# Performance work log

Hardware: AMD Instinct MI355X
Metric: run time of the kernel (lower is better)

The kernel has to match this reference:

```python
import jax, jax.numpy as jnp
import numpy as np

BLOCK = 32          # Q4_0 block size
Q_ZERO = 8.0        # 4-bit zero point


def setup_inputs() -> dict:
    key = jax.random.key(0)
    k1, k2, k3, k4 = jax.random.split(key, 4)
    O, I = 8192, 8192
    nb = I // BLOCK                      # 256 blocks per row
    x = jax.random.normal(k1, (4096, I), dtype=jnp.float32)
    # packed Q4_0 payload: 16 bytes per block, each byte holds two 4-bit quants
    qweight = jax.random.randint(k2, (O, nb, BLOCK // 2), 0, 256, dtype=jnp.int32)
    scales = jax.random.uniform(k3, (O, nb), dtype=jnp.float32)
    bias = jax.random.normal(k4, (O,), dtype=jnp.float32)
    return {"x": x, "qweight": qweight, "scales": scales, "bias": bias}


def _dequantize_q4_0(qweight, scales):
    # qweight: [O, NB, 16] bytes; low nibble -> elems 0..15, high nibble -> 16..31
    O, nb, _ = qweight.shape
    low = qweight & 0xF
    high = (qweight >> 4) & 0xF
    vals = jnp.concatenate([low, high], axis=-1).astype(scales.dtype)  # [O, NB, 32]
    w = (vals - Q_ZERO) * scales[..., None]                            # [O, NB, 32]
    return w.reshape(O, nb * BLOCK)                                    # [O, I]


def reference(x, qweight, scales, bias):
    # GGUFLayer.cast_bias_weight: dequantize weight/bias to input dtype, then linear
    w = _dequantize_q4_0(qweight, scales).astype(x.dtype)  # [O, I]
    b = bias.astype(x.dtype)
    return jnp.einsum('ni,oi->no', x, w) + b               # F.linear(x, w, b)
```

## Files before the change

kernel.cpp:

```cpp
#include <hip/hip_runtime.h>
#include <stdint.h>

#define M_DIM 4096
#define N_DIM 8192
#define K_DIM 8192
#define NB    256

#define BM 256
#define BN 256
#define BK 64

typedef __attribute__((ext_vector_type(8)))  __bf16 bf16x8;
typedef __attribute__((ext_vector_type(16))) float  floatx16;
typedef __attribute__((ext_vector_type(4)))  unsigned short ushort4v;
typedef __attribute__((ext_vector_type(8)))  unsigned short ushort8;

__device__ __forceinline__ unsigned short f32_to_bf16_rne(float f) {
    union { float f; unsigned int u; } v; v.f = f;
    unsigned int u = v.u;
    u += 0x7FFFu + ((u >> 16) & 1u);
    return (unsigned short)(u >> 16);
}

__global__ __launch_bounds__(256) void prep(const int* __restrict__ qw,
                                            const float* __restrict__ sc,
                                            unsigned short* __restrict__ w,
                                            const float* __restrict__ x,
                                            unsigned short* __restrict__ xb) {
    const int bid = blockIdx.x;
    if (bid & 1) {
        size_t idx = ((size_t)(bid >> 1) * 256 + threadIdx.x) * 4;
        float4 f = *(const float4*)(x + idx);
        ushort4v o;
        o[0] = f32_to_bf16_rne(f.x); o[1] = f32_to_bf16_rne(f.y);
        o[2] = f32_to_bf16_rne(f.z); o[3] = f32_to_bf16_rne(f.w);
        *(ushort4v*)(xb + idx) = o;
    } else {
        const int tid = (bid >> 1) * 256 + threadIdx.x;
        const int blk = tid >> 2;
        const int q   = tid & 3;
        const int4* src = (const int4*)qw + (size_t)blk * 4 + (q & 1) * 2;
        int4 v0 = src[0];
        int4 v1 = src[1];
        const float scale = sc[blk];
        const int sh = (q >> 1) * 4;
        int by[8] = { v0.x, v0.y, v0.z, v0.w, v1.x, v1.y, v1.z, v1.w };
        ushort8 o;
#pragma unroll
        for (int j = 0; j < 8; ++j)
            o[j] = f32_to_bf16_rne((float)(((by[j] >> sh) & 0xF) - 8) * scale);
        *(ushort8*)(w + (size_t)blk * 32 + q * 8) = o;
    }
}

__device__ __forceinline__ void load_lds16(const unsigned short* g, unsigned short* l) {
    __builtin_amdgcn_global_load_lds(
        (const __attribute__((address_space(1))) unsigned int*)(g),
        (__attribute__((address_space(3))) unsigned int*)(l),
        16, 0, 0);
}

__device__ __forceinline__ floatx16 mfma_op(bf16x8 a, bf16x8 b, floatx16 c) {
    return __builtin_amdgcn_mfma_f32_32x32x16_bf16(a, b, c, 0, 0, 0);
}

#define SL(kk, F) (((((kk) * 2) + q5) ^ (F)) * 8)

#define STAGE_A(b, h, kb) do { \
    load_lds16(gA + (size_t)((h) * 128 +  0) * K_DIM + (kb) * BK, &lsA[b][((h) * 128 +  0 + wave * 8) * BK]); \
    load_lds16(gA + (size_t)((h) * 128 + 64) * K_DIM + (kb) * BK, &lsA[b][((h) * 128 + 64 + wave * 8) * BK]); \
} while (0)
#define STAGE_B(b, h, kb) do { \
    load_lds16(gB + (size_t)((h) * 128 +  0) * K_DIM + (kb) * BK, &lsB[b][((h) * 128 +  0 + wave * 8) * BK]); \
    load_lds16(gB + (size_t)((h) * 128 + 64) * K_DIM + (kb) * BK, &lsB[b][((h) * 128 + 64 + wave * 8) * BK]); \
} while (0)

#define PH_HEAD __builtin_amdgcn_s_barrier(); \
                asm volatile("s_waitcnt lgkmcnt(0)" ::: "memory"); \
                __builtin_amdgcn_s_setprio(1)
#define PH_TAIL __builtin_amdgcn_s_setprio(0)

#define TILE(bb, S1, S2, S3, S4, VMW) do { \
     \
    _Pragma("unroll") for (int kk = 0; kk < 4; ++kk) { \
        aL[0][kk] = *(const bf16x8*)(&lsA[bb][aA0 + SL(kk, F0)]); \
        aL[1][kk] = *(const bf16x8*)(&lsA[bb][aA1 + SL(kk, F1)]); \
        b0[kk]    = *(const bf16x8*)(&lsB[bb][aB0 + SL(kk, F0)]); \
    } \
    S1; PH_HEAD; \
    _Pragma("unroll") for (int kk = 0; kk < 4; ++kk) { \
        acc[0][0] = mfma_op(aL[0][kk], b0[kk], acc[0][0]); \
        acc[1][0] = mfma_op(aL[1][kk], b0[kk], acc[1][0]); \
    } \
    PH_TAIL; __builtin_amdgcn_s_barrier(); \
     \
    _Pragma("unroll") for (int kk = 0; kk < 4; ++kk) \
        b1[kk] = *(const bf16x8*)(&lsB[bb][aB1 + SL(kk, F1)]); \
    S2; PH_HEAD; \
    _Pragma("unroll") for (int kk = 0; kk < 4; ++kk) { \
        acc[0][1] = mfma_op(aL[0][kk], b1[kk], acc[0][1]); \
        acc[1][1] = mfma_op(aL[1][kk], b1[kk], acc[1][1]); \
    } \
    PH_TAIL; __builtin_amdgcn_s_barrier(); \
     \
    _Pragma("unroll") for (int kk = 0; kk < 4; ++kk) { \
        aH[0][kk] = *(const bf16x8*)(&lsA[bb][aA2 + SL(kk, F0)]); \
        aH[1][kk] = *(const bf16x8*)(&lsA[bb][aA3 + SL(kk, F1)]); \
    } \
    S3; PH_HEAD; \
    _Pragma("unroll") for (int kk = 0; kk < 4; ++kk) { \
        acc[2][0] = mfma_op(aH[0][kk], b0[kk], acc[2][0]); \
        acc[3][0] = mfma_op(aH[1][kk], b0[kk], acc[3][0]); \
    } \
    PH_TAIL; __builtin_amdgcn_s_barrier(); \
     \
    S4; __builtin_amdgcn_s_barrier(); __builtin_amdgcn_s_setprio(1); \
    _Pragma("unroll") for (int kk = 0; kk < 4; ++kk) { \
        acc[2][1] = mfma_op(aH[0][kk], b1[kk], acc[2][1]); \
        acc[3][1] = mfma_op(aH[1][kk], b1[kk], acc[3][1]); \
    } \
    __builtin_amdgcn_s_setprio(0); VMW; __builtin_amdgcn_s_barrier(); \
} while (0)

__global__ __launch_bounds__(512, 2) void gemm_bt(const unsigned short* __restrict__ A,
                                                  const unsigned short* __restrict__ B,
                                                  const float* __restrict__ bias,
                                                  float* __restrict__ C) {
    __shared__ unsigned short lsA[2][BM * BK];
    __shared__ unsigned short lsB[2][BN * BK];

    const int tid  = threadIdx.x;
    const int wave = tid >> 6;
    const int lane = tid & 63;
    const int wm = wave >> 2;
    const int wn = wave & 3;

    const int bid = blockIdx.x;
    const int wg  = (bid & 7) * 64 + (bid >> 3);
    const int m0 = (wg >> 5) * BM;
    const int n0 = (wg & 31) * BN;

    const int lrow = lane >> 3;
    const int l7s  = lane & 7;
    const int csrc = ((l7s ^ lrow ^ wave) & 7) * 8;
    const unsigned short* gA = A + (size_t)(m0 + wave * 8 + lrow) * K_DIM + csrc;
    const unsigned short* gB = B + (size_t)(n0 + wave * 8 + lrow) * K_DIM + csrc;

    const int q5  = lane >> 5;
    const int r31 = lane & 31;
    const int l7  = lane & 7;
    const int rh  = r31 >> 3;
    const int aA0 = (wm * 128 +  0 + r31) * BK;
    const int aA1 = (wm * 128 + 32 + r31) * BK;
    const int aA2 = (wm * 128 + 64 + r31) * BK;
    const int aA3 = (wm * 128 + 96 + r31) * BK;
    const int aB0 = (wn * 64  +  0 + r31) * BK;
    const int aB1 = (wn * 64  + 32 + r31) * BK;
    const int F0  = l7 ^ (rh & 7);
    const int F1  = l7 ^ ((4 + rh) & 7);

    floatx16 acc[2][4];
    floatx16 accT[4][2] = {};
    (void)acc;
    bf16x8 aL[2][4], aH[2][4], b0[4], b1[4];
#define acc accT

    STAGE_B(0, 0, 0); STAGE_B(0, 1, 0);
    STAGE_A(0, 0, 0); STAGE_A(0, 1, 0);
    STAGE_B(1, 0, 1); STAGE_B(1, 1, 1);
    asm volatile("s_waitcnt vmcnt(4)" ::: "memory");
    __builtin_amdgcn_s_barrier();

    for (int i = 0; i < 63; ++i) {
        const int t0 = 2 * i;
        TILE(0, STAGE_A(1, 0, t0 + 1), STAGE_A(1, 1, t0 + 1),
                STAGE_B(0, 0, t0 + 2), STAGE_B(0, 1, t0 + 2),
                asm volatile("s_waitcnt vmcnt(4)" ::: "memory"));
        TILE(1, STAGE_A(0, 0, t0 + 2), STAGE_A(0, 1, t0 + 2),
                STAGE_B(1, 0, t0 + 3), STAGE_B(1, 1, t0 + 3),
                asm volatile("s_waitcnt vmcnt(4)" ::: "memory"));
    }
    TILE(0, STAGE_A(1, 0, 127), STAGE_A(1, 1, 127), (void)0, (void)0,
            asm volatile("s_waitcnt vmcnt(0)" ::: "memory"));
    TILE(1, (void)0, (void)0, (void)0, (void)0, (void)0);

#pragma unroll
    for (int fj = 0; fj < 2; ++fj) {
        const int col = n0 + wn * 64 + fj * 32 + r31;
        const float bv = bias[col];
#pragma unroll
        for (int fi = 0; fi < 4; ++fi) {
            const int rowbase = m0 + wm * 128 + fi * 32 + q5 * 4;
            const floatx16 av = acc[fi][fj];
#pragma unroll
            for (int r = 0; r < 16; ++r) {
                const int row = rowbase + (r & 3) + 8 * (r >> 2);
                C[(size_t)row * N_DIM + col] = av[r] + bv;
            }
        }
    }
#undef acc
}

extern "C" void kernel_launch(void* const* d_in, const int* in_sizes, int n_in,
                              void* d_out, int out_size, void* d_ws, size_t ws_size,
                              hipStream_t stream) {
    (void)in_sizes; (void)n_in; (void)out_size; (void)ws_size;
    const float* x    = (const float*)d_in[0];
    const int*   qw   = (const int*)d_in[1];
    const float* sc   = (const float*)d_in[2];
    const float* bias = (const float*)d_in[3];
    float* out = (float*)d_out;

    unsigned short* Wb = (unsigned short*)d_ws;
    unsigned short* Xb = (unsigned short*)((char*)d_ws + (size_t)N_DIM * K_DIM * 2);

    prep<<<dim3(65536), dim3(256), 0, stream>>>(qw, sc, Wb, x, Xb);
    gemm_bt<<<dim3((M_DIM / BM) * (N_DIM / BN)), dim3(512), 0, stream>>>(Xb, Wb, bias, out);
}
```

Measured before the change: 821.7 us.

## Replace phased ping-pong GEMM schedule with simple double-buffered tile loop

Drops the four-phase per-tile schedule, which interleaved LDS fragment reads, staged global-to-LDS loads and MFMA clusters with several barriers and priority changes. The new loop issues every load for the next tile up front, reads all A/B fragments from LDS, runs all 32 MFMAs at raised priority, then waits for all outstanding loads and synchronises once per tile. This cuts barrier and phase overhead but removes the B prefetch two tiles ahead and the finer overlap between loads and math. Global-load latency is now hidden only by a single tile of compute.

```diff
diff --git a/kernel.cpp b/kernel.cpp
--- a/kernel.cpp
+++ b/kernel.cpp
@@ -74,52 +74,41 @@
     load_lds16(gB + (size_t)((h) * 128 +  0) * K_DIM + (kb) * BK, &lsB[b][((h) * 128 +  0 + wave * 8) * BK]); \
     load_lds16(gB + (size_t)((h) * 128 + 64) * K_DIM + (kb) * BK, &lsB[b][((h) * 128 + 64 + wave * 8) * BK]); \
 } while (0)
+#define STAGE_ALL(dst, kb) do { \
+    STAGE_A(dst, 0, kb); STAGE_A(dst, 1, kb); \
+    STAGE_B(dst, 0, kb); STAGE_B(dst, 1, kb); \
+} while (0)
 
-#define PH_HEAD __builtin_amdgcn_s_barrier(); \
-                asm volatile("s_waitcnt lgkmcnt(0)" ::: "memory"); \
-                __builtin_amdgcn_s_setprio(1)
-#define PH_TAIL __builtin_amdgcn_s_setprio(0)
+#define CL(ai, jj, av, bv) \
+    _Pragma("unroll") for (int kk = 0; kk < 4; ++kk) \
+        acc[ai][jj] = mfma_op(av[kk], bv[kk], acc[ai][jj]);
 
-#define TILE(bb, S1, S2, S3, S4, VMW) do { \
-     \
+#define PRIO1   __builtin_amdgcn_s_setprio(1)
+#define PRIO0   __builtin_amdgcn_s_setprio(0)
+#define BAR     __builtin_amdgcn_s_barrier()
+
+#define TILE_FREE(bb, STAGES, TAILOP) do { \
+    STAGES; \
     _Pragma("unroll") for (int kk = 0; kk < 4; ++kk) { \
+        b0[kk]    = *(const bf16x8*)(&lsB[bb][aB0 + SL(kk, F0)]); \
+        b1[kk]    = *(const bf16x8*)(&lsB[bb][aB1 + SL(kk, F1)]); \
         aL[0][kk] = *(const bf16x8*)(&lsA[bb][aA0 + SL(kk, F0)]); \
         aL[1][kk] = *(const bf16x8*)(&lsA[bb][aA1 + SL(kk, F1)]); \
-        b0[kk]    = *(const bf16x8*)(&lsB[bb][aB0 + SL(kk, F0)]); \
-    } \
-    S1; PH_HEAD; \
-    _Pragma("unroll") for (int kk = 0; kk < 4; ++kk) { \
-        acc[0][0] = mfma_op(aL[0][kk], b0[kk], acc[0][0]); \
-        acc[1][0] = mfma_op(aL[1][kk], b0[kk], acc[1][0]); \
-    } \
-    PH_TAIL; __builtin_amdgcn_s_barrier(); \
-     \
-    _Pragma("unroll") for (int kk = 0; kk < 4; ++kk) \
-        b1[kk] = *(const bf16x8*)(&lsB[bb][aB1 + SL(kk, F1)]); \
-    S2; PH_HEAD; \
-    _Pragma("unroll") for (int kk = 0; kk < 4; ++kk) { \
-        acc[0][1] = mfma_op(aL[0][kk], b1[kk], acc[0][1]); \
-        acc[1][1] = mfma_op(aL[1][kk], b1[kk], acc[1][1]); \
-    } \
-    PH_TAIL; __builtin_amdgcn_s_barrier(); \
-     \
-    _Pragma("unroll") for (int kk = 0; kk < 4; ++kk) { \
         aH[0][kk] = *(const bf16x8*)(&lsA[bb][aA2 + SL(kk, F0)]); \
         aH[1][kk] = *(const bf16x8*)(&lsA[bb][aA3 + SL(kk, F1)]); \
     } \
-    S3; PH_HEAD; \
-    _Pragma("unroll") for (int kk = 0; kk < 4; ++kk) { \
-        acc[2][0] = mfma_op(aH[0][kk], b0[kk], acc[2][0]); \
-        acc[3][0] = mfma_op(aH[1][kk], b0[kk], acc[3][0]); \
-    } \
-    PH_TAIL; __builtin_amdgcn_s_barrier(); \
-     \
-    S4; __builtin_amdgcn_s_barrier(); __builtin_amdgcn_s_setprio(1); \
-    _Pragma("unroll") for (int kk = 0; kk < 4; ++kk) { \
-        acc[2][1] = mfma_op(aH[0][kk], b1[kk], acc[2][1]); \
-        acc[3][1] = mfma_op(aH[1][kk], b1[kk], acc[3][1]); \
-    } \
-    __builtin_amdgcn_s_setprio(0); VMW; __builtin_amdgcn_s_barrier(); \
+    PRIO1; \
+    CL(0, 0, aL[0], b0); CL(1, 0, aL[1], b0); \
+    CL(0, 1, aL[0], b1); CL(1, 1, aL[1], b1); \
+    CL(2, 0, aH[0], b0); CL(3, 0, aH[1], b0); \
+    CL(2, 1, aH[0], b1); CL(3, 1, aH[1], b1); \
+    PRIO0; \
+    TAILOP; \
+} while (0)
+
+#define TILE_TAIL do { \
+    asm volatile("s_waitcnt vmcnt(0)" ::: "memory"); \
+    BAR; \
 } while (0)
 
 __global__ __launch_bounds__(512, 2) void gemm_bt(const unsigned short* __restrict__ A,
@@ -159,30 +148,20 @@
     const int F0  = l7 ^ (rh & 7);
     const int F1  = l7 ^ ((4 + rh) & 7);
 
-    floatx16 acc[2][4];
-    floatx16 accT[4][2] = {};
-    (void)acc;
+    floatx16 acc[4][2] = {};
     bf16x8 aL[2][4], aH[2][4], b0[4], b1[4];
-#define acc accT
 
-    STAGE_B(0, 0, 0); STAGE_B(0, 1, 0);
-    STAGE_A(0, 0, 0); STAGE_A(0, 1, 0);
-    STAGE_B(1, 0, 1); STAGE_B(1, 1, 1);
-    asm volatile("s_waitcnt vmcnt(4)" ::: "memory");
-    __builtin_amdgcn_s_barrier();
+    STAGE_ALL(0, 0);
+    asm volatile("s_waitcnt vmcnt(0)" ::: "memory");
+    BAR;
 
     for (int i = 0; i < 63; ++i) {
         const int t0 = 2 * i;
-        TILE(0, STAGE_A(1, 0, t0 + 1), STAGE_A(1, 1, t0 + 1),
-                STAGE_B(0, 0, t0 + 2), STAGE_B(0, 1, t0 + 2),
-                asm volatile("s_waitcnt vmcnt(4)" ::: "memory"));
-        TILE(1, STAGE_A(0, 0, t0 + 2), STAGE_A(0, 1, t0 + 2),
-                STAGE_B(1, 0, t0 + 3), STAGE_B(1, 1, t0 + 3),
-                asm volatile("s_waitcnt vmcnt(4)" ::: "memory"));
+        TILE_FREE(0, STAGE_ALL(1, t0 + 1), TILE_TAIL);
+        TILE_FREE(1, STAGE_ALL(0, t0 + 2), TILE_TAIL);
     }
-    TILE(0, STAGE_A(1, 0, 127), STAGE_A(1, 1, 127), (void)0, (void)0,
-            asm volatile("s_waitcnt vmcnt(0)" ::: "memory"));
-    TILE(1, (void)0, (void)0, (void)0, (void)0, (void)0);
+    TILE_FREE(0, STAGE_ALL(1, 127), TILE_TAIL);
+    TILE_FREE(1, (void)0, (void)0);
 
 #pragma unroll
     for (int fj = 0; fj < 2; ++fj) {
@@ -199,7 +178,6 @@
             }
         }
     }
-#undef acc
 }
 
 extern "C" void kernel_launch(void* const* d_in, const int* in_sizes, int n_in,
```

Measured after the change: 941.8 us. 1.15x slower.
